# Optimization experiments

Hardware: AMD Instinct MI355X
Metric: run time of the kernel (lower is better)

The kernel has to match this reference:

```python
import jax, jax.numpy as jnp
import numpy as np

N = 8192
F_IN, F_HID, F_OUT = 256, 256, 64


def setup_inputs() -> dict:
    key = jax.random.key(0)
    k1, k2, k3, k4 = jax.random.split(key, 4)
    adj = jax.random.uniform(k1, (N, N), dtype=jnp.float32)
    x = jax.random.normal(k2, (N, F_IN), dtype=jnp.float32)
    W1 = jax.random.uniform(k3, (F_IN, F_HID), dtype=jnp.float32)
    W2 = jax.random.uniform(k4, (F_HID, F_OUT), dtype=jnp.float32)
    return {"adj": adj, "x": x, "W1": W1, "W2": W2}


def reference(adj, x, W1, W2):
    # Layer 1: left_to_right -> (adj @ x) @ W1, then ReLU (dropout is identity in eval)
    h = jnp.matmul(jnp.matmul(adj, x), W1)
    h = jax.nn.relu(h)
    # Layer 2 (last): no activation
    h = jnp.matmul(jnp.matmul(adj, h), W2)
    # Final log_softmax over class dim
    return jax.nn.log_softmax(h, axis=1)
```

## Files before the change

kernel.cpp:

```cpp
#include <hip/hip_runtime.h>

typedef short bf16x8 __attribute__((ext_vector_type(8)));
typedef float f32x4 __attribute__((ext_vector_type(4)));
typedef unsigned short us8 __attribute__((ext_vector_type(8)));

__device__ __forceinline__ unsigned short f2bf(float f) {
    unsigned int u = __float_as_uint(f);
    u += 0x7fffu + ((u >> 16) & 1u);
    return (unsigned short)(u >> 16);
}

__device__ __forceinline__ void hard_barrier() {
    asm volatile("s_waitcnt lgkmcnt(0)" ::: "memory");
    __builtin_amdgcn_sched_barrier(0);
    __builtin_amdgcn_s_barrier();
    __builtin_amdgcn_sched_barrier(0);
}

__global__ __launch_bounds__(256) void transpose_cast_kernel(
    const float* __restrict__ in, unsigned short* __restrict__ out, int R, int Cc) {
    __shared__ alignas(16) unsigned short sT[64][65];
    const int r0 = blockIdx.x * 64, c0 = blockIdx.y * 64;
    const int t = threadIdx.x;
#pragma unroll
    for (int p = 0; p < 16; ++p) {
        int flat = p * 256 + t;
        int r = flat >> 6, c = flat & 63;
        sT[c][r] = f2bf(in[(size_t)(r0 + r) * Cc + (c0 + c)]);
    }
    __syncthreads();
#pragma unroll
    for (int p = 0; p < 16; ++p) {
        int flat = p * 256 + t;
        int c = flat >> 6, r = flat & 63;
        out[(size_t)(c0 + c) * R + (r0 + r)] = sT[c][r];
    }
}

template<int BN, int WM, int WN, int AMODE, bool TOUT, typename OutT>
__global__ __launch_bounds__(256) void gemm_kernel(
    const void* __restrict__ Aptr, const unsigned short* __restrict__ BT,
    OutT* __restrict__ C, int M, int N, int K, long aslab) {
    constexpr int BM = 64, BK = 64, LDW = 72;
    constexpr int MF = BM / WM / 16;
    constexpr int NF = BN / WN / 16;
    __shared__ alignas(16) unsigned short sA[BM * LDW];
    __shared__ alignas(16) unsigned short sB[BN * LDW];
    const int t = threadIdx.x;
    const int w = t >> 6, l = t & 63;
    const int wr = w / WN, wc = w % WN;
    const int m0 = blockIdx.x * BM;

    f32x4 acc[MF][NF] = {};

    for (int k0 = 0; k0 < K; k0 += BK) {
        const float* A32 = (const float*)Aptr;
#pragma unroll
        for (int p = 0; p < 4; ++p) {
            int flat = p * 256 + t;
            int row = flat >> 4, c4 = flat & 15;
            size_t base = (size_t)(m0 + row) * K + k0 + c4 * 4;
            float4 v = *(const float4*)&A32[base];
            if constexpr (AMODE == 2) {
                float4 b = *(const float4*)&A32[aslab + base];
                float4 c = *(const float4*)&A32[2 * aslab + base];
                float4 d = *(const float4*)&A32[3 * aslab + base];
                v.x = fmaxf(v.x + b.x + c.x + d.x, 0.f);
                v.y = fmaxf(v.y + b.y + c.y + d.y, 0.f);
                v.z = fmaxf(v.z + b.z + c.z + d.z, 0.f);
                v.w = fmaxf(v.w + b.w + c.w + d.w, 0.f);
            }
            ushort4 o = make_ushort4(f2bf(v.x), f2bf(v.y), f2bf(v.z), f2bf(v.w));
            *(ushort4*)&sA[row * LDW + c4 * 4] = o;
        }
#pragma unroll
        for (int p = 0; p < BN * 8 / 256; ++p) {
            int flat = p * 256 + t;
            int row = flat >> 3, c8 = flat & 7;
            us8 v = *(const us8*)&BT[(size_t)row * K + k0 + c8 * 8];
            *(us8*)&sB[row * LDW + c8 * 8] = v;
        }
        __syncthreads();
#pragma unroll
        for (int kk = 0; kk < BK; kk += 32) {
            bf16x8 av[MF], bv[NF];
#pragma unroll
            for (int m = 0; m < MF; ++m)
                av[m] = *(const bf16x8*)&sA[(wr * (BM / WM) + m * 16 + (l & 15)) * LDW + kk + (l >> 4) * 8];
#pragma unroll
            for (int n = 0; n < NF; ++n)
                bv[n] = *(const bf16x8*)&sB[(wc * (BN / WN) + n * 16 + (l & 15)) * LDW + kk + (l >> 4) * 8];
#pragma unroll
            for (int m = 0; m < MF; ++m)
#pragma unroll
                for (int n = 0; n < NF; ++n)
                    acc[m][n] = __builtin_amdgcn_mfma_f32_16x16x32_bf16(av[m], bv[n], acc[m][n], 0, 0, 0);
        }
        __syncthreads();
    }

#pragma unroll
    for (int m = 0; m < MF; ++m) {
#pragma unroll
        for (int n = 0; n < NF; ++n) {
            const int col = wc * (BN / WN) + n * 16 + (l & 15);
            const int rb = m0 + wr * (BM / WM) + m * 16 + ((l >> 4) << 2);
            float v0 = acc[m][n][0], v1 = acc[m][n][1], v2 = acc[m][n][2], v3 = acc[m][n][3];
            if constexpr (TOUT) {
                ushort4 o = make_ushort4(f2bf(v0), f2bf(v1), f2bf(v2), f2bf(v3));
                *(ushort4*)((unsigned short*)C + (size_t)col * M + rb) = o;
            } else {
                C[(size_t)(rb + 0) * N + col] = (OutT)v0;
                C[(size_t)(rb + 1) * N + col] = (OutT)v1;
                C[(size_t)(rb + 2) * N + col] = (OutT)v2;
                C[(size_t)(rb + 3) * N + col] = (OutT)v3;
            }
        }
    }
}

template<int BM, int BN, int WM, int WN, int THREADS>
__global__ __launch_bounds__(THREADS, 4) void pipe_gemm_kernel(
    const float* __restrict__ A, const unsigned short* __restrict__ BT,
    float* __restrict__ C, int M, int N, int K) {
    constexpr int BK = 64, LDW = 72;
    constexpr int MF = BM / WM / 16, NF = BN / WN / 16;
    constexpr int ACH = BM * BK / 4 / THREADS;
    constexpr int BCH = BN * BK / 8 / THREADS;
    static_assert(ACH * THREADS * 4 == BM * BK && BCH * THREADS * 8 == BN * BK, "split");
    __shared__ alignas(16) unsigned short sA[2][BM * LDW];
    __shared__ alignas(16) unsigned short sB[2][BN * LDW];
    const int t = threadIdx.x, w = t >> 6, l = t & 63;
    const int wr = w / WN, wc = w % WN;
    const int nx = gridDim.x;
    const int lin = blockIdx.x + nx * blockIdx.z;
    const int cpx = (nx * gridDim.z) >> 3;
    const int sw = (lin & 7) * cpx + (lin >> 3);
    const int bx = sw % nx, bz = sw / nx;
    const int m0 = bx * BM;
    const int klen = K / gridDim.z, kbeg = bz * klen;
    const int NT = klen / BK;
    float* Cp = C + (size_t)bz * M * N;

    float4 a0[ACH], a1[ACH];
    us8 b0[BCH], b1[BCH];

    auto LOAD = [&](float4 (&ar)[ACH], us8 (&br)[BCH], int k0) {
#pragma unroll
        for (int p = 0; p < ACH; ++p) {
            int flat = p * THREADS + t, row = flat >> 4, c4 = flat & 15;
            ar[p] = *(const float4*)&A[(size_t)(m0 + row) * K + k0 + c4 * 4];
        }
#pragma unroll
        for (int p = 0; p < BCH; ++p) {
            int flat = p * THREADS + t, row = flat >> 3, c8 = flat & 7;
            br[p] = *(const us8*)&BT[(size_t)row * K + k0 + c8 * 8];
        }
    };
    auto WRITE = [&](float4 (&ar)[ACH], us8 (&br)[BCH], int buf) {
#pragma unroll
        for (int p = 0; p < ACH; ++p) {
            int flat = p * THREADS + t, row = flat >> 4, c4 = flat & 15;
            float4 v = ar[p];
            *(ushort4*)&sA[buf][row * LDW + c4 * 4] =
                make_ushort4(f2bf(v.x), f2bf(v.y), f2bf(v.z), f2bf(v.w));
        }
#pragma unroll
        for (int p = 0; p < BCH; ++p) {
            int flat = p * THREADS + t, row = flat >> 3, c8 = flat & 7;
            *(us8*)&sB[buf][row * LDW + c8 * 8] = br[p];
        }
    };

    f32x4 acc[MF][NF] = {};

    auto COMPUTE = [&](int buf) {
#pragma unroll
        for (int kk = 0; kk < BK; kk += 32) {
            bf16x8 av[MF], bv[NF];
#pragma unroll
            for (int m = 0; m < MF; ++m)
                av[m] = *(const bf16x8*)&sA[buf][(wr * (BM / WM) + m * 16 + (l & 15)) * LDW + kk + (l >> 4) * 8];
#pragma unroll
            for (int n = 0; n < NF; ++n)
                bv[n] = *(const bf16x8*)&sB[buf][(wc * (BN / WN) + n * 16 + (l & 15)) * LDW + kk + (l >> 4) * 8];
#pragma unroll
            for (int m = 0; m < MF; ++m)
#pragma unroll
                for (int n = 0; n < NF; ++n)
                    acc[m][n] = __builtin_amdgcn_mfma_f32_16x16x32_bf16(av[m], bv[n], acc[m][n], 0, 0, 0);
        }
    };

    LOAD(a0, b0, kbeg);
    LOAD(a1, b1, kbeg + BK);
    WRITE(a0, b0, 0);
    hard_barrier();

    for (int tt = 0; tt < NT; tt += 2) {
        if (tt + 2 < NT) LOAD(a0, b0, kbeg + (tt + 2) * BK);
        __builtin_amdgcn_sched_barrier(0);
        COMPUTE(0);
        if (tt + 1 < NT) WRITE(a1, b1, 1);
        hard_barrier();
        if (tt + 1 < NT) {
            if (tt + 3 < NT) LOAD(a1, b1, kbeg + (tt + 3) * BK);
            __builtin_amdgcn_sched_barrier(0);
            COMPUTE(1);
            if (tt + 2 < NT) WRITE(a0, b0, 0);
            hard_barrier();
        }
    }

#pragma unroll
    for (int m = 0; m < MF; ++m)
#pragma unroll
        for (int n = 0; n < NF; ++n) {
            const int col = wc * (BN / WN) + n * 16 + (l & 15);
            const int rb = m0 + wr * (BM / WM) + m * 16 + ((l >> 4) << 2);
#pragma unroll
            for (int j = 0; j < 4; ++j)
                Cp[(size_t)(rb + j) * N + col] = acc[m][n][j];
        }
}

__global__ __launch_bounds__(256) void head2_kernel(
    const float* __restrict__ p, float* __restrict__ out, int M) {
    const int t = threadIdx.x, w = t >> 6, l = t & 63;
    const size_t stride = (size_t)M * 64;
#pragma unroll
    for (int rr = 0; rr < 4; ++rr) {
        int i = blockIdx.x * 16 + w * 4 + rr;
        size_t off = (size_t)i * 64 + l;
        float v = 0.f;
#pragma unroll
        for (int s = 0; s < 8; ++s) v += p[s * stride + off];
        float mx = v;
#pragma unroll
        for (int o = 32; o; o >>= 1) mx = fmaxf(mx, __shfl_xor(mx, o));
        float d0 = v - mx;
        float e = __expf(d0);
#pragma unroll
        for (int o = 32; o; o >>= 1) e += __shfl_xor(e, o);
        out[off] = d0 - __logf(e);
    }
}

extern "C" void kernel_launch(void* const* d_in, const int* in_sizes, int n_in,
                              void* d_out, int out_size, void* d_ws, size_t ws_size,
                              hipStream_t stream) {
    const float* adj = (const float*)d_in[0];
    const float* x   = (const float*)d_in[1];
    const float* W1  = (const float*)d_in[2];
    const float* W2  = (const float*)d_in[3];
    float* out = (float*)d_out;

    const int M = 8192, K = 8192;
    char* ws = (char*)d_ws;
    float*          pbuf1 = (float*)ws;
    float*          pbuf2 = (float*)(ws + 33554432);
    unsigned short* zT    = (unsigned short*)(ws + 50331648);
    unsigned short* hwT   = (unsigned short*)(ws + 54525952);
    unsigned short* W1T   = (unsigned short*)(ws + 55574528);
    unsigned short* W2T   = (unsigned short*)(ws + 55705600);

    transpose_cast_kernel<<<dim3(4, 4), 256, 0, stream>>>(W1, W1T, 256, 256);
    transpose_cast_kernel<<<dim3(4, 1), 256, 0, stream>>>(W2, W2T, 256, 64);
    gemm_kernel<256, 1, 4, 1, true, unsigned short>
        <<<dim3(M / 64), 256, 0, stream>>>(x, W1T, zT, M, 256, 256, 0);
    pipe_gemm_kernel<128, 256, 4, 4, 1024>
        <<<dim3(M / 128, 1, 4), 1024, 0, stream>>>(adj, zT, pbuf1, M, 256, K);
    gemm_kernel<64, 2, 2, 2, true, unsigned short>
        <<<dim3(M / 64), 256, 0, stream>>>(pbuf1, W2T, hwT, M, 64, 256, (long)M * 256);
    pipe_gemm_kernel<128, 64, 4, 2, 512>
        <<<dim3(M / 128, 1, 8), 512, 0, stream>>>(adj, hwT, pbuf2, M, 64, K);
    head2_kernel<<<dim3(M / 16), 256, 0, stream>>>(pbuf2, out, M);
}
```

Baseline: 157.4 us.

## Retile first adjacency GEMM, split-K by eight, emit bf16 partials

The large adj@z GEMM changes from 1024-thread blocks with BK=64 and 4-way split-K to 512-thread blocks with BK=32, a 2x4 warp grid and 8-way split-K. Its partial results are now stored as bf16, which halves the partial-buffer write and read traffic. The following small GEMM gains a new mode that sums eight bf16 slabs and applies ReLU. The MFMA inner loop now loads one B fragment at a time to reduce register pressure. Rounding each partial to bf16 adds precision loss, and 8-way split-K doubles the number of partial slabs to reduce.

New measurement: 258.6 us. +64.3%, slower.

```diff
diff --git a/kernel.cpp b/kernel.cpp
--- a/kernel.cpp
+++ b/kernel.cpp
@@ -8,6 +8,9 @@
     unsigned int u = __float_as_uint(f);
     u += 0x7fffu + ((u >> 16) & 1u);
     return (unsigned short)(u >> 16);
+}
+__device__ __forceinline__ float bf2f(unsigned short s) {
+    return __uint_as_float((unsigned int)s << 16);
 }
 
 __device__ __forceinline__ void hard_barrier() {
@@ -54,24 +57,35 @@
     f32x4 acc[MF][NF] = {};
 
     for (int k0 = 0; k0 < K; k0 += BK) {
-        const float* A32 = (const float*)Aptr;
-#pragma unroll
-        for (int p = 0; p < 4; ++p) {
-            int flat = p * 256 + t;
-            int row = flat >> 4, c4 = flat & 15;
-            size_t base = (size_t)(m0 + row) * K + k0 + c4 * 4;
-            float4 v = *(const float4*)&A32[base];
-            if constexpr (AMODE == 2) {
-                float4 b = *(const float4*)&A32[aslab + base];
-                float4 c = *(const float4*)&A32[2 * aslab + base];
-                float4 d = *(const float4*)&A32[3 * aslab + base];
-                v.x = fmaxf(v.x + b.x + c.x + d.x, 0.f);
-                v.y = fmaxf(v.y + b.y + c.y + d.y, 0.f);
-                v.z = fmaxf(v.z + b.z + c.z + d.z, 0.f);
-                v.w = fmaxf(v.w + b.w + c.w + d.w, 0.f);
-            }
-            ushort4 o = make_ushort4(f2bf(v.x), f2bf(v.y), f2bf(v.z), f2bf(v.w));
-            *(ushort4*)&sA[row * LDW + c4 * 4] = o;
+        if constexpr (AMODE == 1) {
+            const float* A32 = (const float*)Aptr;
+#pragma unroll
+            for (int p = 0; p < 4; ++p) {
+                int flat = p * 256 + t;
+                int row = flat >> 4, c4 = flat & 15;
+                float4 v = *(const float4*)&A32[(size_t)(m0 + row) * K + k0 + c4 * 4];
+                *(ushort4*)&sA[row * LDW + c4 * 4] =
+                    make_ushort4(f2bf(v.x), f2bf(v.y), f2bf(v.z), f2bf(v.w));
+            }
+        } else {
+            const unsigned short* A16 = (const unsigned short*)Aptr;
+#pragma unroll
+            for (int p = 0; p < 2; ++p) {
+                int flat = p * 256 + t;
+                int row = flat >> 3, c8 = flat & 7;
+                size_t base = (size_t)(m0 + row) * K + k0 + c8 * 8;
+                float s[8] = {};
+#pragma unroll
+                for (int sl = 0; sl < 8; ++sl) {
+                    us8 v = *(const us8*)&A16[(size_t)sl * aslab + base];
+#pragma unroll
+                    for (int e = 0; e < 8; ++e) s[e] += bf2f(v[e]);
+                }
+                us8 o;
+#pragma unroll
+                for (int e = 0; e < 8; ++e) o[e] = f2bf(fmaxf(s[e], 0.f));
+                *(us8*)&sA[row * LDW + c8 * 8] = o;
+            }
         }
 #pragma unroll
         for (int p = 0; p < BN * 8 / 256; ++p) {
@@ -119,12 +133,14 @@
     }
 }
 
-template<int BM, int BN, int WM, int WN, int THREADS>
+template<int BM, int BN, int BK, int WM, int WN, int THREADS, bool OUTBF>
 __global__ __launch_bounds__(THREADS, 4) void pipe_gemm_kernel(
     const float* __restrict__ A, const unsigned short* __restrict__ BT,
-    float* __restrict__ C, int M, int N, int K) {
-    constexpr int BK = 64, LDW = 72;
+    void* __restrict__ Cout, int M, int N, int K) {
+    constexpr int LDW = BK + 8;
     constexpr int MF = BM / WM / 16, NF = BN / WN / 16;
+    constexpr int APR = BK / 4;
+    constexpr int BPR = BK / 8;
     constexpr int ACH = BM * BK / 4 / THREADS;
     constexpr int BCH = BN * BK / 8 / THREADS;
     static_assert(ACH * THREADS * 4 == BM * BK && BCH * THREADS * 8 == BN * BK, "split");
@@ -140,7 +156,6 @@
     const int m0 = bx * BM;
     const int klen = K / gridDim.z, kbeg = bz * klen;
     const int NT = klen / BK;
-    float* Cp = C + (size_t)bz * M * N;
 
     float4 a0[ACH], a1[ACH];
     us8 b0[BCH], b1[BCH];
@@ -148,26 +163,26 @@
     auto LOAD = [&](float4 (&ar)[ACH], us8 (&br)[BCH], int k0) {
 #pragma unroll
         for (int p = 0; p < ACH; ++p) {
-            int flat = p * THREADS + t, row = flat >> 4, c4 = flat & 15;
+            int flat = p * THREADS + t, row = flat / APR, c4 = flat % APR;
             ar[p] = *(const float4*)&A[(size_t)(m0 + row) * K + k0 + c4 * 4];
         }
 #pragma unroll
         for (int p = 0; p < BCH; ++p) {
-            int flat = p * THREADS + t, row = flat >> 3, c8 = flat & 7;
+            int flat = p * THREADS + t, row = flat / BPR, c8 = flat % BPR;
             br[p] = *(const us8*)&BT[(size_t)row * K + k0 + c8 * 8];
         }
     };
     auto WRITE = [&](float4 (&ar)[ACH], us8 (&br)[BCH], int buf) {
 #pragma unroll
         for (int p = 0; p < ACH; ++p) {
-            int flat = p * THREADS + t, row = flat >> 4, c4 = flat & 15;
+            int flat = p * THREADS + t, row = flat / APR, c4 = flat % APR;
             float4 v = ar[p];
             *(ushort4*)&sA[buf][row * LDW + c4 * 4] =
                 make_ushort4(f2bf(v.x), f2bf(v.y), f2bf(v.z), f2bf(v.w));
         }
 #pragma unroll
         for (int p = 0; p < BCH; ++p) {
-            int flat = p * THREADS + t, row = flat >> 3, c8 = flat & 7;
+            int flat = p * THREADS + t, row = flat / BPR, c8 = flat % BPR;
             *(us8*)&sB[buf][row * LDW + c8 * 8] = br[p];
         }
     };
@@ -177,18 +192,17 @@
     auto COMPUTE = [&](int buf) {
 #pragma unroll
         for (int kk = 0; kk < BK; kk += 32) {
-            bf16x8 av[MF], bv[NF];
+            bf16x8 av[MF];
 #pragma unroll
             for (int m = 0; m < MF; ++m)
                 av[m] = *(const bf16x8*)&sA[buf][(wr * (BM / WM) + m * 16 + (l & 15)) * LDW + kk + (l >> 4) * 8];
 #pragma unroll
-            for (int n = 0; n < NF; ++n)
-                bv[n] = *(const bf16x8*)&sB[buf][(wc * (BN / WN) + n * 16 + (l & 15)) * LDW + kk + (l >> 4) * 8];
-#pragma unroll
-            for (int m = 0; m < MF; ++m)
-#pragma unroll
-                for (int n = 0; n < NF; ++n)
-                    acc[m][n] = __builtin_amdgcn_mfma_f32_16x16x32_bf16(av[m], bv[n], acc[m][n], 0, 0, 0);
+            for (int n = 0; n < NF; ++n) {
+                bf16x8 bv = *(const bf16x8*)&sB[buf][(wc * (BN / WN) + n * 16 + (l & 15)) * LDW + kk + (l >> 4) * 8];
+#pragma unroll
+                for (int m = 0; m < MF; ++m)
+                    acc[m][n] = __builtin_amdgcn_mfma_f32_16x16x32_bf16(av[m], bv, acc[m][n], 0, 0, 0);
+            }
         }
     };
 
@@ -219,8 +233,14 @@
             const int col = wc * (BN / WN) + n * 16 + (l & 15);
             const int rb = m0 + wr * (BM / WM) + m * 16 + ((l >> 4) << 2);
 #pragma unroll
-            for (int j = 0; j < 4; ++j)
-                Cp[(size_t)(rb + j) * N + col] = acc[m][n][j];
+            for (int j = 0; j < 4; ++j) {
+                if constexpr (OUTBF)
+                    ((unsigned short*)Cout)[(size_t)bz * M * N + (size_t)(rb + j) * N + col] =
+                        f2bf(acc[m][n][j]);
+                else
+                    ((float*)Cout)[(size_t)bz * M * N + (size_t)(rb + j) * N + col] =
+                        acc[m][n][j];
+            }
         }
 }
 
@@ -257,7 +277,7 @@
 
     const int M = 8192, K = 8192;
     char* ws = (char*)d_ws;
-    float*          pbuf1 = (float*)ws;
+    unsigned short* pbuf1 = (unsigned short*)ws;
     float*          pbuf2 = (float*)(ws + 33554432);
     unsigned short* zT    = (unsigned short*)(ws + 50331648);
     unsigned short* hwT   = (unsigned short*)(ws + 54525952);
@@ -268,11 +288,11 @@
     transpose_cast_kernel<<<dim3(4, 1), 256, 0, stream>>>(W2, W2T, 256, 64);
     gemm_kernel<256, 1, 4, 1, true, unsigned short>
         <<<dim3(M / 64), 256, 0, stream>>>(x, W1T, zT, M, 256, 256, 0);
-    pipe_gemm_kernel<128, 256, 4, 4, 1024>
-        <<<dim3(M / 128, 1, 4), 1024, 0, stream>>>(adj, zT, pbuf1, M, 256, K);
-    gemm_kernel<64, 2, 2, 2, true, unsigned short>
+    pipe_gemm_kernel<128, 256, 32, 2, 4, 512, true>
+        <<<dim3(M / 128, 1, 8), 512, 0, stream>>>(adj, zT, pbuf1, M, 256, K);
+    gemm_kernel<64, 2, 2, 3, true, unsigned short>
         <<<dim3(M / 64), 256, 0, stream>>>(pbuf1, W2T, hwT, M, 64, 256, (long)M * 256);
-    pipe_gemm_kernel<128, 64, 4, 2, 512>
+    pipe_gemm_kernel<128, 64, 64, 4, 2, 512, false>
         <<<dim3(M / 128, 1, 8), 512, 0, stream>>>(adj, hwT, pbuf2, M, 64, K);
     head2_kernel<<<dim3(M / 16), 256, 0, stream>>>(pbuf2, out, M);
 }
```
